# Kernel optimization log

Hardware: AMD Instinct MI355X
Metric: run time of the kernel (lower is better)

Reference implementation:

```python
import jax, jax.numpy as jnp
import numpy as np

N_NODES = 16384
N_EDGES = 262144
N_GRAPHS = 64
COLORS = 16
EMB = 256
HEADS = 8
FFN = 1024
LAYERS = 4
LMAX = 320


def _ln(x, g, b, eps=1e-5):
    m = x.mean(-1, keepdims=True)
    v = x.var(-1, keepdims=True)
    return (x - m) * jax.lax.rsqrt(v + eps) * g + b


def setup_inputs() -> dict:
    key = jax.random.key(0)
    ks = iter(jax.random.split(key, 64))
    s = 0.05
    def rn(shape):
        return jax.random.normal(next(ks), shape, jnp.float32) * s
    # 64 graphs: 32 with 192 nodes, 32 with 320 nodes -> total 16384, L_max=320
    lengths = np.concatenate([np.full(32, 192, np.int64), np.full(32, 320, np.int64)])
    batches = jnp.asarray(np.concatenate([[0], np.cumsum(lengths)]).astype(np.int32))
    x = jax.random.normal(next(ks), (N_NODES, COLORS), jnp.float32)
    edge_index = jax.random.randint(next(ks), (2, N_EDGES), 0, N_NODES, jnp.int32)
    inp = dict(
        x=x, edge_index=edge_index, batches=batches, L_max=LMAX,
        sW0=rn((COLORS, EMB)), sWn0=rn((COLORS, EMB)), sb0=jnp.zeros(EMB),
        sW1=rn((EMB, EMB)), sWn1=rn((EMB, EMB)), sb1=jnp.zeros(EMB),
        sW2=rn((EMB, EMB)), sWn2=rn((EMB, EMB)), sb2=jnp.zeros(EMB),
        Wq=rn((LAYERS, EMB, EMB)), Wk=rn((LAYERS, EMB, EMB)), Wv=rn((LAYERS, EMB, EMB)),
        bq=jnp.zeros((LAYERS, EMB)), bk=jnp.zeros((LAYERS, EMB)), bv=jnp.zeros((LAYERS, EMB)),
        Wo=rn((LAYERS, EMB, EMB)), bo=jnp.zeros((LAYERS, EMB)),
        ln1g=jnp.ones((LAYERS, EMB)), ln1b=jnp.zeros((LAYERS, EMB)),
        ln2g=jnp.ones((LAYERS, EMB)), ln2b=jnp.zeros((LAYERS, EMB)),
        W1=rn((LAYERS, EMB, FFN)), b1=jnp.zeros((LAYERS, FFN)),
        W2=rn((LAYERS, FFN, EMB)), b2=jnp.zeros((LAYERS, EMB)),
    )
    return inp


def reference(x, edge_index, batches, L_max,
              sW0, sWn0, sb0, sW1, sWn1, sb1, sW2, sWn2, sb2,
              Wq, Wk, Wv, bq, bk, bv, Wo, bo,
              ln1g, ln1b, ln2g, ln2b, W1, b1, W2, b2):
    N = x.shape[0]
    src, dst = edge_index[0], edge_index[1]
    deg = jnp.maximum(
        jax.ops.segment_sum(jnp.ones(src.shape[0], x.dtype), dst, num_segments=N), 1.0
    )[:, None]

    def sage(h, Ws, Wn, b, act):
        agg = jax.ops.segment_sum(h[src], dst, num_segments=N) / deg  # mean neighbor agg
        h2 = h @ Ws + agg @ Wn + b
        return jax.nn.relu(h2) if act else h2

    z = sage(x, sW0, sWn0, sb0, True)
    z = sage(z, sW1, sWn1, sb1, True)
    z = sage(z, sW2, sWn2, sb2, False)

    # pack_and_pad (intended semantics): seq-first [L_max, n_graphs, D] + key padding mask
    nG = batches.shape[0] - 1
    lengths = batches[1:] - batches[:-1]
    ids = jnp.arange(N)
    seg = jnp.searchsorted(batches, ids, side='right') - 1  # graph id per node
    pos = ids - batches[seg]                                 # position within graph
    D = z.shape[1]
    h = jnp.zeros((L_max, nG, D), z.dtype).at[pos, seg].set(z)
    pad = jnp.arange(L_max)[None, :] >= lengths[:, None]     # [nG, L_max], True = padded

    H = HEADS
    dh = D // H
    scale = 1.0 / np.sqrt(dh).astype(np.float32)
    for l in range(Wq.shape[0]):
        L, Bg = h.shape[0], h.shape[1]
        q = (h @ Wq[l] + bq[l]).reshape(L, Bg, H, dh)
        k = (h @ Wk[l] + bk[l]).reshape(L, Bg, H, dh)
        v = (h @ Wv[l] + bv[l]).reshape(L, Bg, H, dh)
        sc = jnp.einsum('lbhd,mbhd->bhlm', q, k) * scale
        sc = jnp.where(pad[:, None, None, :], -1e9, sc)
        a = jax.nn.softmax(sc, axis=-1)
        o = jnp.einsum('bhlm,mbhd->lbhd', a, v).reshape(L, Bg, D) @ Wo[l] + bo[l]
        h = _ln(h + o, ln1g[l], ln1b[l])
        ff = jax.nn.relu(h @ W1[l] + b1[l]) @ W2[l] + b2[l]
        h = _ln(h + ff, ln2g[l], ln2b[l])
    return h
```

## Files before the change

### kernel.cpp

```cpp
#include <hip/hip_runtime.h>
#include <hip/hip_bf16.h>
#include <math.h>

#define NN  16384
#define NE  262144
#define NG  64
#define CIN 16
#define DD  256
#define NHD 8
#define DHD 32
#define DFF 1024
#define NLY 4
#define LM  320
#define NR  (LM*NG)
#define QS  768
#define QKW 512

typedef __attribute__((ext_vector_type(8))) short bf16x8;
typedef __attribute__((ext_vector_type(4))) float f32x4;

__device__ __forceinline__ unsigned short f2bf(float f) {
    union { __hip_bfloat16 h; unsigned short u; } cv;
    cv.h = __float2bfloat16(f);
    return cv.u;
}
__device__ __forceinline__ float bf2f(unsigned short u) {
    return __uint_as_float((unsigned int)u << 16);
}
__device__ __forceinline__ void gl_lds16(const unsigned short* g, unsigned short* l) {
    __builtin_amdgcn_global_load_lds(
        (const __attribute__((address_space(1))) unsigned int*)g,
        (__attribute__((address_space(3))) unsigned int*)l, 16, 0, 0);
}

__global__ void zero_ws_kernel(uint4* __restrict__ hb, int n16, int* __restrict__ counts) {
    int i = blockIdx.x * 256 + threadIdx.x;
    if (i < n16) hb[i] = (uint4){0u, 0u, 0u, 0u};
    if (i < NN) counts[i] = 0;
}

__global__ __launch_bounds__(256) void prep_all_kernel(
    const float* __restrict__ Wq, const float* __restrict__ Wk, const float* __restrict__ Wv,
    const float* __restrict__ Wo, const float* __restrict__ W1, const float* __restrict__ W2,
    const float* __restrict__ sW1, const float* __restrict__ sWn1,
    const float* __restrict__ sW2, const float* __restrict__ sWn2,
    const float* __restrict__ bq, const float* __restrict__ bk, const float* __restrict__ bv,
    unsigned short* __restrict__ Wqkvt, unsigned short* __restrict__ Wot,
    unsigned short* __restrict__ W1t, unsigned short* __restrict__ W2t,
    unsigned short* __restrict__ sW1t, unsigned short* __restrict__ sWn1t,
    unsigned short* __restrict__ sW2t, unsigned short* __restrict__ sWn2t,
    float* __restrict__ bqkvp)
{
    const int t = threadIdx.x;
    int bid = blockIdx.x;
    if (bid < 12) {
        int i = bid * 256 + t;
        if (i < NLY * QS) {
            int n = i % QS, l = i / QS;
            const float* b = (n < 256) ? bq : (n < 512 ? bk : bv);
            float v = b[l * DD + (n & 255)];
            if (n < 256) v *= 0.17677669529663687f;
            bqkvp[i] = v;
        }
        return;
    }
    bid -= 12;
    __shared__ float Ls[64][68];
    const float* inP;
    unsigned short* outP;
    int strideIn, strideOut;
    float sc = 1.f;
    if (bid < 192) {
        int x = bid % 12, y = (bid / 12) % 4, l = bid / 48;
        int n0 = x * 64, k0 = y * 64;
        const float* W = (n0 < 256) ? Wq : (n0 < 512 ? Wk : Wv);
        if (n0 < 256) sc = 0.17677669529663687f;
        inP  = W + ((size_t)l * DD + k0) * DD + (n0 & 255);
        strideIn = DD;
        outP = Wqkvt + ((size_t)l * QS + n0) * DD + k0;
        strideOut = DD;
    } else if (bid < 192 + 64) {
        bid -= 192;
        int x = bid % 4, y = (bid / 4) % 4, l = bid / 16;
        int n0 = x * 64, k0 = y * 64;
        inP  = Wo + ((size_t)l * DD + k0) * DD + n0;
        strideIn = DD;
        outP = Wot + ((size_t)l * DD + n0) * DD + k0;
        strideOut = DD;
    } else if (bid < 192 + 64 + 256) {
        bid -= 192 + 64;
        int x = bid % 16, y = (bid / 16) % 4, l = bid / 64;
        int n0 = x * 64, k0 = y * 64;
        inP  = W1 + ((size_t)l * DD + k0) * DFF + n0;
        strideIn = DFF;
        outP = W1t + ((size_t)l * DFF + n0) * DD + k0;
        strideOut = DD;
    } else if (bid < 192 + 64 + 512) {
        bid -= 192 + 64 + 256;
        int x = bid % 4, y = (bid / 4) % 16, l = bid / 64;
        int n0 = x * 64, k0 = y * 64;
        inP  = W2 + ((size_t)l * DFF + k0) * DD + n0;
        strideIn = DD;
        outP = W2t + ((size_t)l * DD + n0) * DFF + k0;
        strideOut = DFF;
    } else {
        bid -= 192 + 64 + 512;
        int w = bid / 16, r = bid % 16;
        int x = r % 4, y = r / 4;
        int n0 = x * 64, k0 = y * 64;
        const float* src = (w == 0) ? sW1 : (w == 1) ? sWn1 : (w == 2) ? sW2 : sWn2;
        unsigned short* dst = (w == 0) ? sW1t : (w == 1) ? sWn1t : (w == 2) ? sW2t : sWn2t;
        inP  = src + (size_t)k0 * DD + n0;
        strideIn = DD;
        outP = dst + (size_t)n0 * DD + k0;
        strideOut = DD;
    }
    #pragma unroll
    for (int it = 0; it < 4; ++it) {
        int lin = it * 256 + t;
        int kr = lin >> 4, nc = (lin & 15) * 4;
        float4 v = *(const float4*)&inP[(size_t)kr * strideIn + nc];
        Ls[kr][nc]     = v.x * sc;
        Ls[kr][nc + 1] = v.y * sc;
        Ls[kr][nc + 2] = v.z * sc;
        Ls[kr][nc + 3] = v.w * sc;
    }
    __syncthreads();
    #pragma unroll
    for (int it = 0; it < 2; ++it) {
        int lin = it * 256 + t;
        int nr = lin >> 3, kc = (lin & 7) * 8;
        unsigned short pk[8];
        #pragma unroll
        for (int j = 0; j < 8; ++j) pk[j] = f2bf(Ls[kc + j][nr]);
        *(uint4*)&outP[(size_t)nr * strideOut + kc] = *(uint4*)pk;
    }
}

__global__ void count_edges_kernel(const int* __restrict__ dst, int* __restrict__ counts) {
    int e = blockIdx.x * 256 + threadIdx.x;
    if (e < NE) atomicAdd(&counts[dst[e]], 1);
}

__global__ __launch_bounds__(1024) void scan_kernel(const int* __restrict__ counts,
                                                    int* __restrict__ offsets,
                                                    int* __restrict__ cursor) {
    __shared__ int part[1024];
    int t = threadIdx.x;
    int base = t * 16;
    int s = 0;
    #pragma unroll
    for (int i = 0; i < 16; ++i) s += counts[base + i];
    part[t] = s;
    __syncthreads();
    for (int off = 1; off < 1024; off <<= 1) {
        int val = (t >= off) ? part[t - off] : 0;
        __syncthreads();
        part[t] += val;
        __syncthreads();
    }
    int run = (t == 0) ? 0 : part[t - 1];
    #pragma unroll
    for (int i = 0; i < 16; ++i) {
        offsets[base + i] = run;
        cursor[base + i]  = run;
        run += counts[base + i];
    }
    if (t == 1023) offsets[NN] = run;
}

__global__ void fill_csr_kernel(const int* __restrict__ src, const int* __restrict__ dst,
                                int* __restrict__ cursor, int* __restrict__ csr) {
    int e = blockIdx.x * 256 + threadIdx.x;
    if (e < NE) {
        int p = atomicAdd(&cursor[dst[e]], 1);
        csr[p] = src[e];
    }
}

__global__ __launch_bounds__(256) void agg_mean16_kernel(
    const float* __restrict__ h, const int* __restrict__ offsets,
    const int* __restrict__ csr, float* __restrict__ out)
{
    int node = blockIdx.x * 16 + (threadIdx.x >> 4);
    int d = threadIdx.x & 15;
    int beg = offsets[node], end = offsets[node + 1];
    float acc = 0.f;
    int e = beg;
    for (; e + 1 < end; e += 2) {
        float v0 = h[(size_t)csr[e] * CIN + d];
        float v1 = h[(size_t)csr[e + 1] * CIN + d];
        acc += v0 + v1;
    }
    if (e < end) acc += h[(size_t)csr[e] * CIN + d];
    int dg = end - beg; if (dg < 1) dg = 1;
    out[(size_t)node * CIN + d] = acc * (1.f / (float)dg);
}

__global__ __launch_bounds__(256) void agg_mean_b_kernel(
    const unsigned short* __restrict__ h, const int* __restrict__ offsets,
    const int* __restrict__ csr, unsigned short* __restrict__ out)
{
    int node = blockIdx.x * 4 + (threadIdx.x >> 6);
    int lane = threadIdx.x & 63;
    int half = lane >> 5;
    int hl   = lane & 31;
    int beg = offsets[node], end = offsets[node + 1];
    float a[8] = {0.f, 0.f, 0.f, 0.f, 0.f, 0.f, 0.f, 0.f};
    int e = beg + half;
    for (; e + 2 < end; e += 4) {
        bf16x8 h0 = *(const bf16x8*)(h + (size_t)csr[e] * DD + hl * 8);
        bf16x8 h1 = *(const bf16x8*)(h + (size_t)csr[e + 2] * DD + hl * 8);
        #pragma unroll
        for (int j = 0; j < 8; ++j) a[j] += bf2f((unsigned short)h0[j]);
        #pragma unroll
        for (int j = 0; j < 8; ++j) a[j] += bf2f((unsigned short)h1[j]);
    }
    if (e < end) {
        bf16x8 h0 = *(const bf16x8*)(h + (size_t)csr[e] * DD + hl * 8);
        #pragma unroll
        for (int j = 0; j < 8; ++j) a[j] += bf2f((unsigned short)h0[j]);
    }
    #pragma unroll
    for (int j = 0; j < 8; ++j) a[j] += __shfl_xor(a[j], 32, 64);
    int dg = end - beg; if (dg < 1) dg = 1;
    float inv = 1.f / (float)dg;
    if (half == 0) {
        unsigned short pk[8];
        #pragma unroll
        for (int j = 0; j < 8; ++j) pk[j] = f2bf(a[j] * inv);
        *(uint4*)(out + (size_t)node * DD + hl * 8) = *(uint4*)pk;
    }
}

template <int ACT, bool DUAL>
__global__ __launch_bounds__(256) void gemm_f32b_kernel(
    const float* __restrict__ A, const float* __restrict__ W,
    const float* __restrict__ A2, const float* __restrict__ W2,
    const float* __restrict__ bias, unsigned short* __restrict__ Cb,
    int M, int N, int K)
{
    __shared__ __align__(16) float As[16][64];
    __shared__ __align__(16) float Ws[16][64];
    const int t  = threadIdx.x;
    const int tx = t & 15, ty = t >> 4;
    const int m0 = blockIdx.y * 64, n0 = blockIdx.x * 64;
    const int arow = t >> 2, acol = (t & 3) * 4;
    const int wrow = t >> 4, wcol = (t & 15) * 4;
    float acc[4][4] = {};
    const int npass = DUAL ? 2 : 1;
    for (int pass = 0; pass < npass; ++pass) {
        const float* Ap = (DUAL && pass) ? A2 : A;
        const float* Wp = (DUAL && pass) ? W2 : W;
        for (int k0 = 0; k0 < K; k0 += 16) {
            __syncthreads();
            float4 av = *(const float4*)(Ap + (size_t)(m0 + arow) * K + k0 + acol);
            As[acol + 0][arow] = av.x;
            As[acol + 1][arow] = av.y;
            As[acol + 2][arow] = av.z;
            As[acol + 3][arow] = av.w;
            *(float4*)&Ws[wrow][wcol] = *(const float4*)(Wp + (size_t)(k0 + wrow) * N + n0 + wcol);
            __syncthreads();
            #pragma unroll
            for (int kk = 0; kk < 16; ++kk) {
                float4 a4 = *(const float4*)&As[kk][ty * 4];
                float4 b4 = *(const float4*)&Ws[kk][tx * 4];
                float aa[4] = {a4.x, a4.y, a4.z, a4.w};
                float bb[4] = {b4.x, b4.y, b4.z, b4.w};
                #pragma unroll
                for (int i = 0; i < 4; ++i)
                    #pragma unroll
                    for (int j = 0; j < 4; ++j)
                        acc[i][j] += aa[i] * bb[j];
            }
        }
    }
    float4 bv = *(const float4*)(bias + n0 + tx * 4);
    float bb4[4] = {bv.x, bv.y, bv.z, bv.w};
    #pragma unroll
    for (int i = 0; i < 4; ++i) {
        float c[4];
        #pragma unroll
        for (int j = 0; j < 4; ++j) {
            c[j] = acc[i][j] + bb4[j];
            if (ACT == 1) c[j] = fmaxf(c[j], 0.f);
        }
        ushort4 ov;
        ov.x = f2bf(c[0]); ov.y = f2bf(c[1]); ov.z = f2bf(c[2]); ov.w = f2bf(c[3]);
        *(ushort4*)(Cb + (size_t)(m0 + ty * 4 + i) * N + n0 + tx * 4) = ov;
    }
}

template <int ACT, bool DUAL, bool OUTF32, bool OUTBF16>
__global__ __launch_bounds__(256) void mfma_gemm_kernel(
    const unsigned short* __restrict__ A,  const unsigned short* __restrict__ Wt,
    const unsigned short* __restrict__ A2, const unsigned short* __restrict__ Wt2,
    const float* __restrict__ bias, float* __restrict__ Cf,
    unsigned short* __restrict__ Cb, int M, int N, int K)
{
    __shared__ __align__(16) unsigned short As[128 * 64];
    __shared__ __align__(16) unsigned short Bs[128 * 64];
    const int t = threadIdx.x;
    const int wave = t >> 6, lane = t & 63;
    const int quad = lane >> 4, r16 = lane & 15;
    const int wr = (wave >> 1) * 64, wc = (wave & 1) * 64;
    const int m0 = blockIdx.y * 128, n0 = blockIdx.x * 128;
    const int srow = t >> 3;
    const int scol = ((t & 7) * 8) ^ ((srow & 7) << 3);
    const int swz  = (r16 & 7) << 3;

    f32x4 acc[4][4];
    #pragma unroll
    for (int i = 0; i < 4; ++i)
        #pragma unroll
        for (int j = 0; j < 4; ++j)
            acc[i][j] = (f32x4){0.f, 0.f, 0.f, 0.f};

    const int npass = DUAL ? 2 : 1;
    for (int pass = 0; pass < npass; ++pass) {
        const unsigned short* Ap = (DUAL && pass) ? A2 : A;
        const unsigned short* Wp = (DUAL && pass) ? Wt2 : Wt;
        for (int k0 = 0; k0 < K; k0 += 64) {
            __syncthreads();
            #pragma unroll
            for (int c = 0; c < 4; ++c) {
                gl_lds16(&Ap[(size_t)(m0 + c * 32 + srow) * K + k0 + scol],
                         As + c * 2048 + wave * 512);
                gl_lds16(&Wp[(size_t)(n0 + c * 32 + srow) * K + k0 + scol],
                         Bs + c * 2048 + wave * 512);
            }
            __syncthreads();
            #pragma unroll
            for (int kk = 0; kk < 2; ++kk) {
                const int cofs = (kk * 32 + quad * 8) ^ swz;
                bf16x8 af[4], bfr[4];
                #pragma unroll
                for (int i = 0; i < 4; ++i)
                    af[i] = *(const bf16x8*)&As[(wr + i * 16 + r16) * 64 + cofs];
                #pragma unroll
                for (int j = 0; j < 4; ++j)
                    bfr[j] = *(const bf16x8*)&Bs[(wc + j * 16 + r16) * 64 + cofs];
                #pragma unroll
                for (int i = 0; i < 4; ++i)
                    #pragma unroll
                    for (int j = 0; j < 4; ++j)
                        acc[i][j] = __builtin_amdgcn_mfma_f32_16x16x32_bf16(
                            af[i], bfr[j], acc[i][j], 0, 0, 0);
            }
        }
    }

    float bcol[4];
    #pragma unroll
    for (int j = 0; j < 4; ++j) bcol[j] = bias[n0 + wc + j * 16 + r16];
    #pragma unroll
    for (int i = 0; i < 4; ++i) {
        const int rowb = m0 + wr + i * 16 + quad * 4;
        #pragma unroll
        for (int rr = 0; rr < 4; ++rr) {
            const size_t rb = (size_t)(rowb + rr) * N;
            #pragma unroll
            for (int j = 0; j < 4; ++j) {
                float v = acc[i][j][rr] + bcol[j];
                if (ACT == 1) v = fmaxf(v, 0.f);
                const int col = n0 + wc + j * 16 + r16;
                if (OUTF32) Cf[rb + col] = v;
                if (OUTBF16) Cb[rb + col] = f2bf(v);
            }
        }
    }
}

__global__ __launch_bounds__(256) void gemm_qkv_kernel(
    const unsigned short* __restrict__ A, const unsigned short* __restrict__ Wt,
    const float* __restrict__ bias, unsigned short* __restrict__ QKb,
    unsigned short* __restrict__ Vt, int K)
{
    __shared__ __align__(16) unsigned short As[128 * 64];
    __shared__ __align__(16) unsigned short Bs[128 * 64];
    const int t = threadIdx.x;
    const int wave = t >> 6, lane = t & 63;
    const int quad = lane >> 4, r16 = lane & 15;
    const int wr = (wave >> 1) * 64, wc = (wave & 1) * 64;
    const int m0 = blockIdx.y * 128, n0 = blockIdx.x * 128;
    const int srow = t >> 3;
    const int scol = ((t & 7) * 8) ^ ((srow & 7) << 3);
    const int swz  = (r16 & 7) << 3;

    f32x4 acc[4][4];
    #pragma unroll
    for (int i = 0; i < 4; ++i)
        #pragma unroll
        for (int j = 0; j < 4; ++j)
            acc[i][j] = (f32x4){0.f, 0.f, 0.f, 0.f};

    for (int k0 = 0; k0 < K; k0 += 64) {
        __syncthreads();
        #pragma unroll
        for (int c = 0; c < 4; ++c) {
            gl_lds16(&A[(size_t)(m0 + c * 32 + srow) * K + k0 + scol],
                     As + c * 2048 + wave * 512);
            gl_lds16(&Wt[(size_t)(n0 + c * 32 + srow) * K + k0 + scol],
                     Bs + c * 2048 + wave * 512);
        }
        __syncthreads();
        #pragma unroll
        for (int kk = 0; kk < 2; ++kk) {
            const int cofs = (kk * 32 + quad * 8) ^ swz;
            bf16x8 af[4], bfr[4];
            #pragma unroll
            for (int i = 0; i < 4; ++i)
                af[i] = *(const bf16x8*)&As[(wr + i * 16 + r16) * 64 + cofs];
            #pragma unroll
            for (int j = 0; j < 4; ++j)
                bfr[j] = *(const bf16x8*)&Bs[(wc + j * 16 + r16) * 64 + cofs];
            #pragma unroll
            for (int i = 0; i < 4; ++i)
                #pragma unroll
                for (int j = 0; j < 4; ++j)
                    acc[i][j] = __builtin_amdgcn_mfma_f32_16x16x32_bf16(
                        af[i], bfr[j], acc[i][j], 0, 0, 0);
        }
    }

    float bcol[4];
    #pragma unroll
    for (int j = 0; j < 4; ++j) bcol[j] = bias[n0 + wc + j * 16 + r16];

    if (n0 < 512) {
        #pragma unroll
        for (int i = 0; i < 4; ++i) {
            const int rowb = m0 + wr + i * 16 + quad * 4;
            #pragma unroll
            for (int rr = 0; rr < 4; ++rr) {
                const size_t rb = (size_t)(rowb + rr) * QKW;
                #pragma unroll
                for (int j = 0; j < 4; ++j)
                    QKb[rb + n0 + wc + j * 16 + r16] = f2bf(acc[i][j][rr] + bcol[j]);
            }
        }
    } else {
        #pragma unroll
        for (int i = 0; i < 4; ++i) {
            const int rowb = m0 + wr + i * 16 + quad * 4;
            const int g = rowb / LM;
            const int key = rowb - g * LM;
            #pragma unroll
            for (int j = 0; j < 4; ++j) {
                const int dim = n0 - 512 + wc + j * 16 + r16;
                unsigned short pk[4];
                #pragma unroll
                for (int rr = 0; rr < 4; ++rr) pk[rr] = f2bf(acc[i][j][rr] + bcol[j]);
                *(uint2*)&Vt[((size_t)g * DD + dim) * LM + key] = *(uint2*)pk;
            }
        }
    }
}

template <bool PERM>
__global__ __launch_bounds__(512) void gemm_ln_kernel(
    const unsigned short* __restrict__ A, const unsigned short* __restrict__ Wt,
    const float* __restrict__ bias, const unsigned short* __restrict__ residb,
    const float* __restrict__ gam, const float* __restrict__ bet,
    float* __restrict__ outF, unsigned short* __restrict__ outHb, int K)
{
    __shared__ __align__(16) unsigned short As[64 * 64];
    __shared__ __align__(16) unsigned short Bs[256 * 64];
    __shared__ float red[2][4][64];
    const int t = threadIdx.x;
    const int wave = t >> 6, lane = t & 63;
    const int quad = lane >> 4, r16 = lane & 15;
    const int wr = (wave >> 2) * 32;
    const int wc = (wave & 3) * 64;
    const int m0 = blockIdx.x * 64;
    const int srow = t >> 3;
    const int scol = ((t & 7) * 8) ^ ((srow & 7) << 3);
    const int swz  = (r16 & 7) << 3;

    f32x4 acc[2][4];
    #pragma unroll
    for (int i = 0; i < 2; ++i)
        #pragma unroll
        for (int j = 0; j < 4; ++j)
            acc[i][j] = (f32x4){0.f, 0.f, 0.f, 0.f};

    for (int k0 = 0; k0 < K; k0 += 64) {
        __syncthreads();
        gl_lds16(&A[(size_t)(m0 + srow) * K + k0 + scol], As + wave * 512);
        #pragma unroll
        for (int c = 0; c < 4; ++c)
            gl_lds16(&Wt[(size_t)(c * 64 + srow) * K + k0 + scol],
                     Bs + c * 4096 + wave * 512);
        __syncthreads();
        #pragma unroll
        for (int kk = 0; kk < 2; ++kk) {
            const int cofs = (kk * 32 + quad * 8) ^ swz;
            bf16x8 af[2], bfr[4];
            #pragma unroll
            for (int i = 0; i < 2; ++i)
                af[i] = *(const bf16x8*)&As[(wr + i * 16 + r16) * 64 + cofs];
            #pragma unroll
            for (int j = 0; j < 4; ++j)
                bfr[j] = *(const bf16x8*)&Bs[(wc + j * 16 + r16) * 64 + cofs];
            #pragma unroll
            for (int i = 0; i < 2; ++i)
                #pragma unroll
                for (int j = 0; j < 4; ++j)
                    acc[i][j] = __builtin_amdgcn_mfma_f32_16x16x32_bf16(
                        af[i], bfr[j], acc[i][j], 0, 0, 0);
        }
    }

    float bcol[4];
    #pragma unroll
    for (int j = 0; j < 4; ++j) bcol[j] = bias[wc + j * 16 + r16];

    #pragma unroll
    for (int i = 0; i < 2; ++i) {
        const int row = wr + i * 16 + quad * 4;
        #pragma unroll
        for (int rr = 0; rr < 4; ++rr) {
            const size_t rb = (size_t)(m0 + row + rr) * DD;
            float s1 = 0.f, s2 = 0.f;
            #pragma unroll
            for (int j = 0; j < 4; ++j) {
                float v = acc[i][j][rr] + bcol[j] + bf2f(residb[rb + wc + j * 16 + r16]);
                acc[i][j][rr] = v;
                s1 += v;
                s2 += v * v;
            }
            #pragma unroll
            for (int off = 1; off < 16; off <<= 1) {
                s1 += __shfl_xor(s1, off, 64);
                s2 += __shfl_xor(s2, off, 64);
            }
            if (r16 == 0) {
                red[0][wave & 3][row + rr] = s1;
                red[1][wave & 3][row + rr] = s2;
            }
        }
    }
    __syncthreads();
    #pragma unroll
    for (int i = 0; i < 2; ++i) {
        const int row = wr + i * 16 + quad * 4;
        #pragma unroll
        for (int rr = 0; rr < 4; ++rr) {
            const int lr = row + rr;
            const int gr = m0 + lr;
            float s1 = red[0][0][lr] + red[0][1][lr] + red[0][2][lr] + red[0][3][lr];
            float s2 = red[1][0][lr] + red[1][1][lr] + red[1][2][lr] + red[1][3][lr];
            float mean = s1 * (1.f / 256.f);
            float var  = s2 * (1.f / 256.f) - mean * mean;
            float rs = rsqrtf(var + 1e-5f);
            const size_t hb = (size_t)gr * DD;
            size_t fb = 0;
            if (PERM) {
                int gg = gr / LM, pos = gr - gg * LM;
                fb = ((size_t)pos * NG + gg) * DD;
            }
            #pragma unroll
            for (int j = 0; j < 4; ++j) {
                const int col = wc + j * 16 + r16;
                float ov = (acc[i][j][rr] - mean) * rs * gam[col] + bet[col];
                if (PERM) outF[fb + col] = ov;
                else      outHb[hb + col] = f2bf(ov);
            }
        }
    }
}

__global__ __launch_bounds__(256) void pack_kernel(
    const float* __restrict__ z, const int* __restrict__ batches,
    unsigned short* __restrict__ Hb)
{
    int node = blockIdx.x * 4 + (threadIdx.x >> 6);
    int lane = threadIdx.x & 63;
    int lo = 0, hi = NG;
    while (lo < hi) {
        int mid = (lo + hi + 1) >> 1;
        if (batches[mid] <= node) lo = mid; else hi = mid - 1;
    }
    int pos = node - batches[lo];
    size_t base = ((size_t)lo * LM + pos) * DD + lane * 4;
    float4 zv = *(const float4*)(z + (size_t)node * DD + lane * 4);
    ushort4 hb;
    hb.x = f2bf(zv.x); hb.y = f2bf(zv.y); hb.z = f2bf(zv.z); hb.w = f2bf(zv.w);
    *(ushort4*)(Hb + base) = hb;
}

__global__ __launch_bounds__(256) void attn_mfma_kernel(
    const unsigned short* __restrict__ qk, const unsigned short* __restrict__ vt,
    const int* __restrict__ batches, unsigned short* __restrict__ o)
{
    __shared__ __align__(16) unsigned short Pa[4][64 * 40];
    const int bx = blockIdx.x;
    const int g = bx & 63;
    const int r = bx >> 6;
    const int q0 = (r >> 1) * 64;
    const int tid = threadIdx.x;
    const int wave = tid >> 6;
    const int h = (r & 1) * 4 + wave;
    const int lane = tid & 63;
    const int quad = lane >> 4, r16 = lane & 15;
    const int len = batches[g + 1] - batches[g];
    const size_t gq = (size_t)g * LM;
    unsigned short* pa = Pa[wave];

    bf16x8 qf[4];
    #pragma unroll
    for (int i = 0; i < 4; ++i)
        qf[i] = *(const bf16x8*)(qk + (gq + q0 + i * 16 + r16) * QKW + h * 32 + quad * 8);
    bf16x8 onesf;
    #pragma unroll
    for (int j = 0; j < 8; ++j) onesf[j] = (short)0x3F80;

    f32x4 oacc[4][2], lacc[4];
    #pragma unroll
    for (int i = 0; i < 4; ++i) {
        lacc[i] = (f32x4){0.f, 0.f, 0.f, 0.f};
        #pragma unroll
        for (int nt = 0; nt < 2; ++nt)
            oacc[i][nt] = (f32x4){0.f, 0.f, 0.f, 0.f};
    }

    for (int t0 = 0; t0 < len; t0 += 32) {
        bf16x8 kf[2], vf[2];
        #pragma unroll
        for (int mt = 0; mt < 2; ++mt) {
            int kr = t0 + mt * 16 + r16; if (kr > LM - 1) kr = LM - 1;
            kf[mt] = *(const bf16x8*)(qk + (gq + kr) * QKW + 256 + h * 32 + quad * 8);
        }
        #pragma unroll
        for (int nt = 0; nt < 2; ++nt)
            vf[nt] = *(const bf16x8*)(vt + ((size_t)g * DD + h * 32 + nt * 16 + r16) * LM
                                      + t0 + quad * 8);
        f32x4 st[2][4];
        #pragma unroll
        for (int mt = 0; mt < 2; ++mt)
            #pragma unroll
            for (int i = 0; i < 4; ++i)
                st[mt][i] = (f32x4){0.f, 0.f, 0.f, 0.f};
        #pragma unroll
        for (int mt = 0; mt < 2; ++mt)
            #pragma unroll
            for (int i = 0; i < 4; ++i)
                st[mt][i] = __builtin_amdgcn_mfma_f32_16x16x32_bf16(
                    kf[mt], qf[i], st[mt][i], 0, 0, 0);
        #pragma unroll
        for (int i = 0; i < 4; ++i) {
            #pragma unroll
            for (int mt = 0; mt < 2; ++mt) {
                float pr[4];
                #pragma unroll
                for (int rr = 0; rr < 4; ++rr) {
                    int key = t0 + mt * 16 + quad * 4 + rr;
                    pr[rr] = (key < len) ? __expf(st[mt][i][rr]) : 0.f;
                }
                uint2 w;
                w.x = ((unsigned)f2bf(pr[1]) << 16) | f2bf(pr[0]);
                w.y = ((unsigned)f2bf(pr[3]) << 16) | f2bf(pr[2]);
                *(uint2*)&pa[(i * 16 + r16) * 40 + mt * 16 + quad * 4] = w;
            }
        }
        __asm__ volatile("s_waitcnt lgkmcnt(0)" ::: "memory");
        bf16x8 pf[4];
        #pragma unroll
        for (int i = 0; i < 4; ++i)
            pf[i] = *(const bf16x8*)&pa[(i * 16 + r16) * 40 + quad * 8];
        #pragma unroll
        for (int i = 0; i < 4; ++i) {
            #pragma unroll
            for (int nt = 0; nt < 2; ++nt)
                oacc[i][nt] = __builtin_amdgcn_mfma_f32_16x16x32_bf16(
                    pf[i], vf[nt], oacc[i][nt], 0, 0, 0);
            lacc[i] = __builtin_amdgcn_mfma_f32_16x16x32_bf16(
                pf[i], onesf, lacc[i], 0, 0, 0);
        }
    }
    #pragma unroll
    for (int i = 0; i < 4; ++i) {
        #pragma unroll
        for (int rr = 0; rr < 4; ++rr) {
            float inv = 1.f / lacc[i][rr];
            size_t base = (gq + q0 + i * 16 + quad * 4 + rr) * DD + h * 32;
            #pragma unroll
            for (int nt = 0; nt < 2; ++nt)
                o[base + nt * 16 + r16] = f2bf(oacc[i][nt][rr] * inv);
        }
    }
}

extern "C" void kernel_launch(void* const* d_in, const int* in_sizes, int n_in,
                              void* d_out, int out_size, void* d_ws, size_t ws_size,
                              hipStream_t stream) {
    const float* x       = (const float*)d_in[0];
    const int*   ei      = (const int*)d_in[1];
    const int*   batches = (const int*)d_in[2];
    const float* sW0  = (const float*)d_in[4];
    const float* sWn0 = (const float*)d_in[5];
    const float* sb0  = (const float*)d_in[6];
    const float* sW1  = (const float*)d_in[7];
    const float* sWn1 = (const float*)d_in[8];
    const float* sb1  = (const float*)d_in[9];
    const float* sW2  = (const float*)d_in[10];
    const float* sWn2 = (const float*)d_in[11];
    const float* sb2  = (const float*)d_in[12];
    const float* Wq   = (const float*)d_in[13];
    const float* Wk   = (const float*)d_in[14];
    const float* Wv   = (const float*)d_in[15];
    const float* bq   = (const float*)d_in[16];
    const float* bk   = (const float*)d_in[17];
    const float* bv   = (const float*)d_in[18];
    const float* Wo   = (const float*)d_in[19];
    const float* bo   = (const float*)d_in[20];
    const float* ln1g = (const float*)d_in[21];
    const float* ln1b = (const float*)d_in[22];
    const float* ln2g = (const float*)d_in[23];
    const float* ln2b = (const float*)d_in[24];
    const float* W1   = (const float*)d_in[25];
    const float* b1   = (const float*)d_in[26];
    const float* W2   = (const float*)d_in[27];
    const float* b2   = (const float*)d_in[28];

    char* p = (char*)d_ws;
    auto alloc = [&](size_t bytes) {
        char* r = p;
        p += (bytes + 255) & ~(size_t)255;
        return r;
    };
    int*   counts  = (int*)alloc((size_t)NN * 4);
    int*   offsets = (int*)alloc((size_t)(NN + 1) * 4);
    int*   cursor  = (int*)alloc((size_t)NN * 4);
    int*   csr     = (int*)alloc((size_t)NE * 4);
    float* agg0    = (float*)alloc((size_t)NN * CIN * 4);
    unsigned short* z0b = (unsigned short*)alloc((size_t)NN * DD * 2);
    unsigned short* a1b = (unsigned short*)alloc((size_t)NN * DD * 2);
    unsigned short* z1b = (unsigned short*)alloc((size_t)NN * DD * 2);
    unsigned short* a2b = (unsigned short*)alloc((size_t)NN * DD * 2);
    float* z2f     = (float*)alloc((size_t)NN * DD * 4);
    unsigned short* Vt = (unsigned short*)z2f;
    unsigned short* Hb = (unsigned short*)alloc((size_t)NR * DD * 2);
    unsigned short* Ob = (unsigned short*)alloc((size_t)NR * DD * 2);
    float* R       = (float*)alloc((size_t)NR * DFF * 2);
    unsigned short* QKb = (unsigned short*)R;
    unsigned short* F1b = (unsigned short*)R;
    unsigned short* Wqkvt = (unsigned short*)alloc((size_t)NLY * QS * DD * 2);
    unsigned short* Wot   = (unsigned short*)alloc((size_t)NLY * DD * DD * 2);
    unsigned short* W1t   = (unsigned short*)alloc((size_t)NLY * DFF * DD * 2);
    unsigned short* W2t   = (unsigned short*)alloc((size_t)NLY * DD * DFF * 2);
    unsigned short* sW1t  = (unsigned short*)alloc((size_t)DD * DD * 2);
    unsigned short* sWn1t = (unsigned short*)alloc((size_t)DD * DD * 2);
    unsigned short* sW2t  = (unsigned short*)alloc((size_t)DD * DD * 2);
    unsigned short* sWn2t = (unsigned short*)alloc((size_t)DD * DD * 2);
    float* bqkvp   = (float*)alloc((size_t)NLY * QS * 4);

    prep_all_kernel<<<844, 256, 0, stream>>>(
        Wq, Wk, Wv, Wo, W1, W2, sW1, sWn1, sW2, sWn2, bq, bk, bv,
        Wqkvt, Wot, W1t, W2t, sW1t, sWn1t, sW2t, sWn2t, bqkvp);
    zero_ws_kernel<<<(NR * DD / 8 + 255) / 256, 256, 0, stream>>>(
        (uint4*)Hb, NR * DD / 8, counts);

    count_edges_kernel<<<NE / 256, 256, 0, stream>>>(ei + NE, counts);
    scan_kernel<<<1, 1024, 0, stream>>>(counts, offsets, cursor);
    fill_csr_kernel<<<NE / 256, 256, 0, stream>>>(ei, ei + NE, cursor, csr);

    agg_mean16_kernel<<<NN / 16, 256, 0, stream>>>(x, offsets, csr, agg0);
    gemm_f32b_kernel<1, true><<<dim3(DD / 64, NN / 64), 256, 0, stream>>>(
        x, sW0, agg0, sWn0, sb0, z0b, NN, DD, CIN);
    agg_mean_b_kernel<<<NN / 4, 256, 0, stream>>>(z0b, offsets, csr, a1b);
    mfma_gemm_kernel<1, true, false, true><<<dim3(DD / 128, NN / 128), 256, 0, stream>>>(
        z0b, sW1t, a1b, sWn1t, sb1, nullptr, z1b, NN, DD, DD);
    agg_mean_b_kernel<<<NN / 4, 256, 0, stream>>>(z1b, offsets, csr, a2b);
    mfma_gemm_kernel<0, true, true, false><<<dim3(DD / 128, NN / 128), 256, 0, stream>>>(
        z1b, sW2t, a2b, sWn2t, sb2, z2f, nullptr, NN, DD, DD);

    pack_kernel<<<NN / 4, 256, 0, stream>>>(z2f, batches, Hb);

    for (int l = 0; l < NLY; ++l) {
        gemm_qkv_kernel<<<dim3(QS / 128, NR / 128), 256, 0, stream>>>(
            Hb, Wqkvt + (size_t)l * QS * DD, bqkvp + (size_t)l * QS, QKb, Vt, DD);
        attn_mfma_kernel<<<NG * 10, 256, 0, stream>>>(QKb, Vt, batches, Ob);
        gemm_ln_kernel<false><<<NR / 64, 512, 0, stream>>>(
            Ob, Wot + (size_t)l * DD * DD, bo + (size_t)l * DD, Hb,
            ln1g + (size_t)l * DD, ln1b + (size_t)l * DD, nullptr, Hb, DD);
        mfma_gemm_kernel<1, false, false, true><<<dim3(DFF / 128, NR / 128), 256, 0, stream>>>(
            Hb, W1t + (size_t)l * DFF * DD, nullptr, nullptr,
            b1 + (size_t)l * DFF, nullptr, F1b, NR, DFF, DD);
        if (l == NLY - 1)
            gemm_ln_kernel<true><<<NR / 64, 512, 0, stream>>>(
                F1b, W2t + (size_t)l * DD * DFF, b2 + (size_t)l * DD, Hb,
                ln2g + (size_t)l * DD, ln2b + (size_t)l * DD, (float*)d_out, Hb, DFF);
        else
            gemm_ln_kernel<false><<<NR / 64, 512, 0, stream>>>(
                F1b, W2t + (size_t)l * DD * DFF, b2 + (size_t)l * DD, Hb,
                ln2g + (size_t)l * DD, ln2b + (size_t)l * DD, nullptr, Hb, DFF);
    }
}
```

Measured before the change: 702.2 us.

## Compact transformer rows to real nodes and compute padded rows once per graph

After: 683.5 us. -2.7%, faster.

```diff
diff --git a/kernel.cpp b/kernel.cpp
--- a/kernel.cpp
+++ b/kernel.cpp
@@ -12,9 +12,10 @@
 #define DFF 1024
 #define NLY 4
 #define LM  320
-#define NR  (LM*NG)
 #define QS  768
 #define QKW 512
+#define NV  16384
+#define NRV 16512
 
 typedef __attribute__((ext_vector_type(8))) short bf16x8;
 typedef __attribute__((ext_vector_type(4))) float f32x4;
@@ -32,10 +33,22 @@
         (const __attribute__((address_space(1))) unsigned int*)g,
         (__attribute__((address_space(3))) unsigned int*)l, 16, 0, 0);
 }
-
-__global__ void zero_ws_kernel(uint4* __restrict__ hb, int n16, int* __restrict__ counts) {
+__device__ __forceinline__ int gsearch(const int* __restrict__ batches, int row) {
+    int lo = 0, hi = NG;
+    while (lo < hi) {
+        int mid = (lo + hi + 1) >> 1;
+        if (batches[mid] <= row) lo = mid; else hi = mid - 1;
+    }
+    return lo;
+}
+
+__global__ void zero_ws_kernel(uint4* __restrict__ hbp, uint4* __restrict__ obp,
+                               int* __restrict__ counts) {
     int i = blockIdx.x * 256 + threadIdx.x;
-    if (i < n16) hb[i] = (uint4){0u, 0u, 0u, 0u};
+    if (i < 4096) {
+        hbp[i] = (uint4){0u, 0u, 0u, 0u};
+        obp[i] = (uint4){0u, 0u, 0u, 0u};
+    }
     if (i < NN) counts[i] = 0;
 }
 
@@ -291,12 +304,12 @@
     }
 }
 
-template <int ACT, bool DUAL, bool OUTF32, bool OUTBF16>
+template <int ACT, bool DUAL>
 __global__ __launch_bounds__(256) void mfma_gemm_kernel(
     const unsigned short* __restrict__ A,  const unsigned short* __restrict__ Wt,
     const unsigned short* __restrict__ A2, const unsigned short* __restrict__ Wt2,
-    const float* __restrict__ bias, float* __restrict__ Cf,
-    unsigned short* __restrict__ Cb, int M, int N, int K)
+    const float* __restrict__ bias, unsigned short* __restrict__ Cb,
+    int M, int N, int K)
 {
     __shared__ __align__(16) unsigned short As[128 * 64];
     __shared__ __align__(16) unsigned short Bs[128 * 64];
@@ -363,9 +376,7 @@
             for (int j = 0; j < 4; ++j) {
                 float v = acc[i][j][rr] + bcol[j];
                 if (ACT == 1) v = fmaxf(v, 0.f);
-                const int col = n0 + wc + j * 16 + r16;
-                if (OUTF32) Cf[rb + col] = v;
-                if (OUTBF16) Cb[rb + col] = f2bf(v);
+                Cb[rb + n0 + wc + j * 16 + r16] = f2bf(v);
             }
         }
     }
@@ -373,8 +384,8 @@
 
 __global__ __launch_bounds__(256) void gemm_qkv_kernel(
     const unsigned short* __restrict__ A, const unsigned short* __restrict__ Wt,
-    const float* __restrict__ bias, unsigned short* __restrict__ QKb,
-    unsigned short* __restrict__ Vt, int K)
+    const float* __restrict__ bias, const int* __restrict__ batches,
+    unsigned short* __restrict__ QKb, unsigned short* __restrict__ Vt, int K)
 {
     __shared__ __align__(16) unsigned short As[128 * 64];
     __shared__ __align__(16) unsigned short Bs[128 * 64];
@@ -443,8 +454,9 @@
         #pragma unroll
         for (int i = 0; i < 4; ++i) {
             const int rowb = m0 + wr + i * 16 + quad * 4;
-            const int g = rowb / LM;
-            const int key = rowb - g * LM;
+            if (rowb >= NV) continue;
+            const int g = gsearch(batches, rowb);
+            const int key = rowb - batches[g];
             #pragma unroll
             for (int j = 0; j < 4; ++j) {
                 const int dim = n0 - 512 + wc + j * 16 + r16;
@@ -462,7 +474,9 @@
     const unsigned short* __restrict__ A, const unsigned short* __restrict__ Wt,
     const float* __restrict__ bias, const unsigned short* __restrict__ residb,
     const float* __restrict__ gam, const float* __restrict__ bet,
-    float* __restrict__ outF, unsigned short* __restrict__ outHb, int K)
+    const int* __restrict__ batches,
+    float* __restrict__ outF, float* __restrict__ repO,
+    unsigned short* __restrict__ outHb, int K)
 {
     __shared__ __align__(16) unsigned short As[64 * 64];
     __shared__ __align__(16) unsigned short Bs[256 * 64];
@@ -541,6 +555,12 @@
         }
     }
     __syncthreads();
+
+    int gg = 0, posb = 0;
+    if (PERM && m0 < NV) {
+        gg = gsearch(batches, m0);
+        posb = m0 - batches[gg];
+    }
     #pragma unroll
     for (int i = 0; i < 2; ++i) {
         const int row = wr + i * 16 + quad * 4;
@@ -554,39 +574,23 @@
             float var  = s2 * (1.f / 256.f) - mean * mean;
             float rs = rsqrtf(var + 1e-5f);
             const size_t hb = (size_t)gr * DD;
-            size_t fb = 0;
-            if (PERM) {
-                int gg = gr / LM, pos = gr - gg * LM;
-                fb = ((size_t)pos * NG + gg) * DD;
-            }
             #pragma unroll
             for (int j = 0; j < 4; ++j) {
                 const int col = wc + j * 16 + r16;
                 float ov = (acc[i][j][rr] - mean) * rs * gam[col] + bet[col];
-                if (PERM) outF[fb + col] = ov;
-                else      outHb[hb + col] = f2bf(ov);
-            }
-        }
-    }
-}
-
-__global__ __launch_bounds__(256) void pack_kernel(
-    const float* __restrict__ z, const int* __restrict__ batches,
-    unsigned short* __restrict__ Hb)
-{
-    int node = blockIdx.x * 4 + (threadIdx.x >> 6);
-    int lane = threadIdx.x & 63;
-    int lo = 0, hi = NG;
-    while (lo < hi) {
-        int mid = (lo + hi + 1) >> 1;
-        if (batches[mid] <= node) lo = mid; else hi = mid - 1;
-    }
-    int pos = node - batches[lo];
-    size_t base = ((size_t)lo * LM + pos) * DD + lane * 4;
-    float4 zv = *(const float4*)(z + (size_t)node * DD + lane * 4);
-    ushort4 hb;
-    hb.x = f2bf(zv.x); hb.y = f2bf(zv.y); hb.z = f2bf(zv.z); hb.w = f2bf(zv.w);
-    *(ushort4*)(Hb + base) = hb;
+                if (PERM) {
+                    if (m0 < NV) {
+                        outF[((size_t)(posb + lr) * NG + gg) * DD + col] = ov;
+                    } else {
+                        int g2 = m0 - NV + lr;
+                        if (g2 < NG) repO[(size_t)g2 * DD + col] = ov;
+                    }
+                } else {
+                    outHb[hb + col] = f2bf(ov);
+                }
+            }
+        }
+    }
 }
 
 __global__ __launch_bounds__(256) void attn_mfma_kernel(
@@ -595,22 +599,22 @@
 {
     __shared__ __align__(16) unsigned short Pa[4][64 * 40];
     const int bx = blockIdx.x;
-    const int g = bx & 63;
-    const int r = bx >> 6;
-    const int q0 = (r >> 1) * 64;
+    const int tile = bx >> 1;
+    const int row0 = tile * 64;
     const int tid = threadIdx.x;
     const int wave = tid >> 6;
-    const int h = (r & 1) * 4 + wave;
+    const int h = (bx & 1) * 4 + wave;
     const int lane = tid & 63;
     const int quad = lane >> 4, r16 = lane & 15;
+    const int g = gsearch(batches, row0);
     const int len = batches[g + 1] - batches[g];
-    const size_t gq = (size_t)g * LM;
+    const size_t gq = (size_t)batches[g];
     unsigned short* pa = Pa[wave];
 
     bf16x8 qf[4];
     #pragma unroll
     for (int i = 0; i < 4; ++i)
-        qf[i] = *(const bf16x8*)(qk + (gq + q0 + i * 16 + r16) * QKW + h * 32 + quad * 8);
+        qf[i] = *(const bf16x8*)(qk + (size_t)(row0 + i * 16 + r16) * QKW + h * 32 + quad * 8);
     bf16x8 onesf;
     #pragma unroll
     for (int j = 0; j < 8; ++j) onesf[j] = (short)0x3F80;
@@ -627,10 +631,8 @@
     for (int t0 = 0; t0 < len; t0 += 32) {
         bf16x8 kf[2], vf[2];
         #pragma unroll
-        for (int mt = 0; mt < 2; ++mt) {
-            int kr = t0 + mt * 16 + r16; if (kr > LM - 1) kr = LM - 1;
-            kf[mt] = *(const bf16x8*)(qk + (gq + kr) * QKW + 256 + h * 32 + quad * 8);
-        }
+        for (int mt = 0; mt < 2; ++mt)
+            kf[mt] = *(const bf16x8*)(qk + (gq + t0 + mt * 16 + r16) * QKW + 256 + h * 32 + quad * 8);
         #pragma unroll
         for (int nt = 0; nt < 2; ++nt)
             vf[nt] = *(const bf16x8*)(vt + ((size_t)g * DD + h * 32 + nt * 16 + r16) * LM
@@ -653,10 +655,8 @@
             for (int mt = 0; mt < 2; ++mt) {
                 float pr[4];
                 #pragma unroll
-                for (int rr = 0; rr < 4; ++rr) {
-                    int key = t0 + mt * 16 + quad * 4 + rr;
-                    pr[rr] = (key < len) ? __expf(st[mt][i][rr]) : 0.f;
-                }
+                for (int rr = 0; rr < 4; ++rr)
+                    pr[rr] = __expf(st[mt][i][rr]);
                 uint2 w;
                 w.x = ((unsigned)f2bf(pr[1]) << 16) | f2bf(pr[0]);
                 w.y = ((unsigned)f2bf(pr[3]) << 16) | f2bf(pr[2]);
@@ -683,12 +683,75 @@
         #pragma unroll
         for (int rr = 0; rr < 4; ++rr) {
             float inv = 1.f / lacc[i][rr];
-            size_t base = (gq + q0 + i * 16 + quad * 4 + rr) * DD + h * 32;
+            size_t base = (size_t)(row0 + i * 16 + quad * 4 + rr) * DD + h * 32;
             #pragma unroll
             for (int nt = 0; nt < 2; ++nt)
                 o[base + nt * 16 + r16] = f2bf(oacc[i][nt][rr] * inv);
         }
     }
+}
+
+__global__ __launch_bounds__(256) void attn_rep_kernel(
+    const unsigned short* __restrict__ qk, const unsigned short* __restrict__ vt,
+    const int* __restrict__ batches, unsigned short* __restrict__ o)
+{
+    __shared__ float pbuf[4][LM];
+    const int wave = threadIdx.x >> 6, lane = threadIdx.x & 63;
+    const int idx = blockIdx.x * 4 + wave;
+    const int g = idx >> 3, h = idx & 7;
+    const int len = batches[g + 1] - batches[g];
+    const size_t gq = (size_t)batches[g];
+
+    float q[32];
+    const unsigned short* qrow = qk + (size_t)(NV + g) * QKW + h * 32;
+    #pragma unroll
+    for (int c = 0; c < 4; ++c) {
+        bf16x8 qv = *(const bf16x8*)(qrow + c * 8);
+        #pragma unroll
+        for (int j = 0; j < 8; ++j) q[c * 8 + j] = bf2f((unsigned short)qv[j]);
+    }
+
+    float psum = 0.f;
+    for (int key = lane; key < len; key += 64) {
+        const unsigned short* krow = qk + (gq + key) * QKW + 256 + h * 32;
+        float s = 0.f;
+        #pragma unroll
+        for (int c = 0; c < 4; ++c) {
+            bf16x8 kv = *(const bf16x8*)(krow + c * 8);
+            #pragma unroll
+            for (int j = 0; j < 8; ++j) s += q[c * 8 + j] * bf2f((unsigned short)kv[j]);
+        }
+        float p = __expf(s);
+        pbuf[wave][key] = p;
+        psum += p;
+    }
+    #pragma unroll
+    for (int off = 1; off < 64; off <<= 1) psum += __shfl_xor(psum, off, 64);
+    __syncthreads();
+
+    const int d = lane & 31, half = lane >> 5;
+    float acc = 0.f;
+    const unsigned short* vrow = vt + ((size_t)g * DD + h * 32 + d) * LM;
+    for (int key = half * 8; key < len; key += 16) {
+        bf16x8 v8 = *(const bf16x8*)(vrow + key);
+        #pragma unroll
+        for (int j = 0; j < 8; ++j) acc += pbuf[wave][key + j] * bf2f((unsigned short)v8[j]);
+    }
+    acc += __shfl_xor(acc, 32, 64);
+    if (half == 0)
+        o[(size_t)(NV + g) * DD + h * 32 + d] = f2bf(acc / psum);
+}
+
+__global__ __launch_bounds__(256) void bcast_pad_kernel(
+    const float* __restrict__ repO, const int* __restrict__ batches,
+    float* __restrict__ outF)
+{
+    const int g = blockIdx.x;
+    const int t = threadIdx.x;
+    const int len = batches[g + 1] - batches[g];
+    float v = repO[(size_t)g * DD + t];
+    for (int pos = len; pos < LM; ++pos)
+        outF[((size_t)pos * NG + g) * DD + t] = v;
 }
 
 extern "C" void kernel_launch(void* const* d_in, const int* in_sizes, int n_in,
@@ -738,13 +801,12 @@
     unsigned short* a1b = (unsigned short*)alloc((size_t)NN * DD * 2);
     unsigned short* z1b = (unsigned short*)alloc((size_t)NN * DD * 2);
     unsigned short* a2b = (unsigned short*)alloc((size_t)NN * DD * 2);
-    float* z2f     = (float*)alloc((size_t)NN * DD * 4);
-    unsigned short* Vt = (unsigned short*)z2f;
-    unsigned short* Hb = (unsigned short*)alloc((size_t)NR * DD * 2);
-    unsigned short* Ob = (unsigned short*)alloc((size_t)NR * DD * 2);
-    float* R       = (float*)alloc((size_t)NR * DFF * 2);
-    unsigned short* QKb = (unsigned short*)R;
-    unsigned short* F1b = (unsigned short*)R;
+    unsigned short* Vt = (unsigned short*)alloc((size_t)NG * DD * LM * 2);
+    unsigned short* Hb = (unsigned short*)alloc((size_t)NRV * DD * 2);
+    unsigned short* Ob = (unsigned short*)alloc((size_t)NRV * DD * 2);
+    unsigned short* R  = (unsigned short*)alloc((size_t)NRV * DFF * 2);
+    unsigned short* QKb = R;
+    unsigned short* F1b = R;
     unsigned short* Wqkvt = (unsigned short*)alloc((size_t)NLY * QS * DD * 2);
     unsigned short* Wot   = (unsigned short*)alloc((size_t)NLY * DD * DD * 2);
     unsigned short* W1t   = (unsigned short*)alloc((size_t)NLY * DFF * DD * 2);
@@ -754,12 +816,13 @@
     unsigned short* sW2t  = (unsigned short*)alloc((size_t)DD * DD * 2);
     unsigned short* sWn2t = (unsigned short*)alloc((size_t)DD * DD * 2);
     float* bqkvp   = (float*)alloc((size_t)NLY * QS * 4);
+    float* repOut  = (float*)alloc((size_t)NG * DD * 4);
 
     prep_all_kernel<<<844, 256, 0, stream>>>(
         Wq, Wk, Wv, Wo, W1, W2, sW1, sWn1, sW2, sWn2, bq, bk, bv,
         Wqkvt, Wot, W1t, W2t, sW1t, sWn1t, sW2t, sWn2t, bqkvp);
-    zero_ws_kernel<<<(NR * DD / 8 + 255) / 256, 256, 0, stream>>>(
-        (uint4*)Hb, NR * DD / 8, counts);
+    zero_ws_kernel<<<NN / 256, 256, 0, stream>>>(
+        (uint4*)(Hb + (size_t)NV * DD), (uint4*)(Ob + (size_t)NV * DD), counts);
 
     count_edges_kernel<<<NE / 256, 256, 0, stream>>>(ei + NE, counts);
     scan_kernel<<<1, 1024, 0, stream>>>(counts, offsets, cursor);
@@ -769,31 +832,33 @@
     gemm_f32b_kernel<1, true><<<dim3(DD / 64, NN / 64), 256, 0, stream>>>(
         x, sW0, agg0, sWn0, sb0, z0b, NN, DD, CIN);
     agg_mean_b_kernel<<<NN / 4, 256, 0, stream>>>(z0b, offsets, csr, a1b);
-    mfma_gemm_kernel<1, true, false, true><<<dim3(DD / 128, NN / 128), 256, 0, stream>>>(
-        z0b, sW1t, a1b, sWn1t, sb1, nullptr, z1b, NN, DD, DD);
+    mfma_gemm_kernel<1, true><<<dim3(DD / 128, NN / 128), 256, 0, stream>>>(
+        z0b, sW1t, a1b, sWn1t, sb1, z1b, NN, DD, DD);
     agg_mean_b_kernel<<<NN / 4, 256, 0, stream>>>(z1b, offsets, csr, a2b);
-    mfma_gemm_kernel<0, true, true, false><<<dim3(DD / 128, NN / 128), 256, 0, stream>>>(
-        z1b, sW2t, a2b, sWn2t, sb2, z2f, nullptr, NN, DD, DD);
-
-    pack_kernel<<<NN / 4, 256, 0, stream>>>(z2f, batches, Hb);
+    mfma_gemm_kernel<0, true><<<dim3(DD / 128, NN / 128), 256, 0, stream>>>(
+        z1b, sW2t, a2b, sWn2t, sb2, Hb, NN, DD, DD);
 
     for (int l = 0; l < NLY; ++l) {
-        gemm_qkv_kernel<<<dim3(QS / 128, NR / 128), 256, 0, stream>>>(
-            Hb, Wqkvt + (size_t)l * QS * DD, bqkvp + (size_t)l * QS, QKb, Vt, DD);
-        attn_mfma_kernel<<<NG * 10, 256, 0, stream>>>(QKb, Vt, batches, Ob);
-        gemm_ln_kernel<false><<<NR / 64, 512, 0, stream>>>(
+        gemm_qkv_kernel<<<dim3(QS / 128, NRV / 128), 256, 0, stream>>>(
+            Hb, Wqkvt + (size_t)l * QS * DD, bqkvp + (size_t)l * QS, batches, QKb, Vt, DD);
+        attn_mfma_kernel<<<(NV / 64) * 2, 256, 0, stream>>>(QKb, Vt, batches, Ob);
+        attn_rep_kernel<<<NG * NHD / 4, 256, 0, stream>>>(QKb, Vt, batches, Ob);
+        gemm_ln_kernel<false><<<NRV / 64, 512, 0, stream>>>(
             Ob, Wot + (size_t)l * DD * DD, bo + (size_t)l * DD, Hb,
-            ln1g + (size_t)l * DD, ln1b + (size_t)l * DD, nullptr, Hb, DD);
-        mfma_gemm_kernel<1, false, false, true><<<dim3(DFF / 128, NR / 128), 256, 0, stream>>>(
+            ln1g + (size_t)l * DD, ln1b + (size_t)l * DD, batches, nullptr, nullptr, Hb, DD);
+        mfma_gemm_kernel<1, false><<<dim3(DFF / 128, NRV / 128), 256, 0, stream>>>(
             Hb, W1t + (size_t)l * DFF * DD, nullptr, nullptr,
-            b1 + (size_t)l * DFF, nullptr, F1b, NR, DFF, DD);
+            b1 + (size_t)l * DFF, F1b, NRV, DFF, DD);
         if (l == NLY - 1)
-            gemm_ln_kernel<true><<<NR / 64, 512, 0, stream>>>(
+            gemm_ln_kernel<true><<<NRV / 64, 512, 0, stream>>>(
                 F1b, W2t + (size_t)l * DD * DFF, b2 + (size_t)l * DD, Hb,
-                ln2g + (size_t)l * DD, ln2b + (size_t)l * DD, (float*)d_out, Hb, DFF);
+                ln2g + (size_t)l * DD, ln2b + (size_t)l * DD, batches,
+                (float*)d_out, repOut, Hb, DFF);
         else
-            gemm_ln_kernel<false><<<NR / 64, 512, 0, stream>>>(
+            gemm_ln_kernel<false><<<NRV / 64, 512, 0, stream>>>(
                 F1b, W2t + (size_t)l * DD * DFF, b2 + (size_t)l * DD, Hb,
-                ln2g + (size_t)l * DD, ln2b + (size_t)l * DD, nullptr, Hb, DFF);
-    }
-}
+                ln2g + (size_t)l * DD, ln2b + (size_t)l * DD, batches,
+                nullptr, nullptr, Hb, DFF);
+    }
+    bcast_pad_kernel<<<NG, 256, 0, stream>>>(repOut, batches, (float*)d_out);
+}
```
